# Optimization experiments

Measured on AMD Instinct MI355X. Metric: run time of the kernel, lower is better.

## Reference

```python
import jax, jax.numpy as jnp
import numpy as np

N, F, RBF, E = 50000, 128, 20, 800000
LOG2 = float(np.log(2.0))

def setup_inputs() -> dict:
    key = jax.random.key(0)
    ks = jax.random.split(key, 12)
    s = jax.random.normal(ks[0], (N, F), dtype=jnp.float32)
    v = jax.random.normal(ks[1], (N, F, 3), dtype=jnp.float32)
    edge_index = jax.random.randint(ks[2], (2, E), 0, N, dtype=jnp.int32)
    e_ij = jax.random.uniform(ks[3], (E, RBF), dtype=jnp.float32)
    r = jax.random.normal(ks[4], (E, 3), dtype=jnp.float32)
    r_hat = r / jnp.linalg.norm(r, axis=-1, keepdims=True)
    sc = 1.0 / np.sqrt(F)
    phi_W = jax.random.normal(ks[5], (F, 3 * F), dtype=jnp.float32) * sc
    phi_b = jax.random.normal(ks[6], (3 * F,), dtype=jnp.float32) * 0.01
    f1_W = jax.random.normal(ks[7], (RBF, F), dtype=jnp.float32) * (1.0 / np.sqrt(RBF))
    f1_b = jax.random.normal(ks[8], (F,), dtype=jnp.float32) * 0.01
    f2_W = jax.random.normal(ks[9], (F, 3 * F), dtype=jnp.float32) * sc
    f2_b = jax.random.normal(ks[10], (3 * F,), dtype=jnp.float32) * 0.01
    return {"s": s, "v": v, "e_ij": e_ij, "r_hat": r_hat,
            "phi_W": phi_W, "phi_b": phi_b, "f1_W": f1_W, "f1_b": f1_b,
            "f2_W": f2_W, "f2_b": f2_b, "edge_index": edge_index}

def reference(s, v, e_ij, r_hat, phi_W, phi_b, f1_W, f1_b, f2_W, f2_b, edge_index):
    src, dst = edge_index[0], edge_index[1]
    n = s.shape[0]
    # filter_net: Linear -> shifted softplus -> Linear, per edge
    h = jax.nn.softplus(e_ij @ f1_W + f1_b) - LOG2          # (E, F)
    filt = h @ f2_W + f2_b                                   # (E, 3F)
    W_s, W_v, W_r = jnp.split(filt, 3, axis=-1)              # (E, F) each
    # phi_net on gathered destination scalar features
    phi = s[dst] @ phi_W + phi_b                             # (E, 3F)
    phi_s, phi_v, phi_r = jnp.split(phi, 3, axis=-1)         # (E, F) each
    m_s = W_s * phi_s                                        # (E, F)
    m_v = W_v[..., None] * v[dst] + (W_r * phi_r)[..., None] * r_hat[:, None, :]  # (E, F, 3)
    delta_s = jax.ops.segment_sum(m_s, src, num_segments=n)  # (N, F)
    delta_v = jax.ops.segment_sum(m_v, src, num_segments=n)  # (N, F, 3)
    return delta_s, delta_v
```

## Files before the change

### kernel.cpp

```cpp
#include <hip/hip_runtime.h>
#include <math.h>

#define NN   50000
#define FF   128
#define RBFD 20
#define EE   800000
#define C3F  384
#define TE   32
#define TN   16
#define TEH  64
#define KC   16
#define HP   36

typedef __attribute__((ext_vector_type(8))) short bhalf8;
typedef __attribute__((ext_vector_type(4))) float floatx4;

__device__ __forceinline__ float softplus_m_log2(float x) {
  float t = __expf(-fabsf(x));
  return fmaxf(x, 0.0f) + __logf(1.0f + t) - 0.6931471805599453f;
}

__device__ __forceinline__ short f2bf(float x) {
  unsigned u = __float_as_uint(x);
  u += 0x7fffu + ((u >> 16) & 1u);
  return (short)(u >> 16);
}
__device__ __forceinline__ float bflo(unsigned u) { return __uint_as_float(u << 16); }
__device__ __forceinline__ float bfhi(unsigned u) { return __uint_as_float(u & 0xffff0000u); }

__device__ __forceinline__ int pkf(int f) {
  return ((f >> 5) << 5) | ((f & 15) << 1) | ((f >> 4) & 1);
}

__global__ void hist_kernel(const int* __restrict__ edge_index, int* __restrict__ cursor) {
  int e = blockIdx.x * 256 + threadIdx.x;
  if (e < EE) atomicAdd(&cursor[edge_index[e]], 1);
}

__global__ void scan_kernel(int* __restrict__ cursor, int* __restrict__ row_start) {
  __shared__ int sums[1024];
  const int tid = threadIdx.x;
  const int CH = 49;
  int base = tid * CH;
  int vals[CH];
  int local = 0;
#pragma unroll
  for (int j = 0; j < CH; ++j) {
    int i = base + j;
    int x = (i < NN) ? cursor[i] : 0;
    vals[j] = x;
    local += x;
  }
  sums[tid] = local;
  __syncthreads();
  for (int off = 1; off < 1024; off <<= 1) {
    int v2 = (tid >= off) ? sums[tid - off] : 0;
    __syncthreads();
    sums[tid] += v2;
    __syncthreads();
  }
  int excl = sums[tid] - local;
#pragma unroll
  for (int j = 0; j < CH; ++j) {
    int i = base + j;
    if (i < NN) { row_start[i] = excl; cursor[i] = excl; }
    excl += vals[j];
  }
  if (tid == 1023) row_start[NN] = excl;
}

__global__ void fill_kernel(const int* __restrict__ edge_index, int* __restrict__ cursor,
                            int* __restrict__ perm) {
  int e = blockIdx.x * 256 + threadIdx.x;
  if (e < EE) {
    int s = edge_index[e];
    int pos = atomicAdd(&cursor[s], 1);
    perm[pos] = e;
  }
}

__global__ void fill2_kernel(const int* __restrict__ edge_index, int* __restrict__ cursor,
                             int* __restrict__ perm, int* __restrict__ dst_perm) {
  int e = blockIdx.x * 256 + threadIdx.x;
  if (e < EE) {
    int s = edge_index[e];
    int d = edge_index[EE + e];
    int pos = atomicAdd(&cursor[s], 1);
    perm[pos] = e;
    dst_perm[pos] = d;
  }
}

__global__ void rperm_kernel(const float* __restrict__ r_hat, const int* __restrict__ perm,
                             float* __restrict__ rhp) {
  int i = blockIdx.x * 256 + threadIdx.x;
  if (i < EE) {
    int e = perm[i];
    rhp[(size_t)i * 3 + 0] = r_hat[(size_t)e * 3 + 0];
    rhp[(size_t)i * 3 + 1] = r_hat[(size_t)e * 3 + 1];
    rhp[(size_t)i * 3 + 2] = r_hat[(size_t)e * 3 + 2];
  }
}

__global__ void conv_kernel(const float* __restrict__ f1_W, const float* __restrict__ f2_W,
                            short* __restrict__ f1t, short* __restrict__ f2t) {
  int i = blockIdx.x * 256 + threadIdx.x;
  if (i < C3F * FF) {
    int n = i >> 7, k = i & 127;
    f2t[i] = f2bf(f2_W[(size_t)k * C3F + n]);
  }
  if (i < FF * 40) {
    int f = i / 40, k = i - f * 40;
    f1t[i] = (k < RBFD) ? f2bf(f1_W[(size_t)k * FF + f]) : (short)0;
  }
}

__global__ void vconv_kernel(const float* __restrict__ v, short* __restrict__ v_b16) {
  int i = blockIdx.x * 256 + threadIdx.x;
  if (i < NN * FF * 3) {
    int n = i / 384;
    int rem = i - n * 384;
    int f = rem / 3;
    int c = rem - f * 3;
    int g = f >> 5, l = f & 15, h = (f >> 4) & 1;
    v_b16[(size_t)n * 384 + g * 96 + l * 6 + c * 2 + h] = f2bf(v[i]);
  }
}

__global__ __launch_bounds__(256, 2)
void phi_kernel(const float* __restrict__ s, const float* __restrict__ phi_W,
                const float* __restrict__ phi_b, short* __restrict__ phi_b16) {
  __shared__ float s_t[FF * HP];
  __shared__ __align__(16) float w_ch[KC * 256];
  const int tid = threadIdx.x;
  const int r0 = blockIdx.x * TE;

  for (int i = tid; i < TE * (FF / 4); i += 256) {
    int row = i >> 5, k4 = i & 31;
    int rg = r0 + row;
    float4 sv = make_float4(0.f, 0.f, 0.f, 0.f);
    if (rg < NN) sv = *(const float4*)(s + (size_t)rg * FF + k4 * 4);
    s_t[(k4 * 4 + 0) * HP + row] = sv.x;
    s_t[(k4 * 4 + 1) * HP + row] = sv.y;
    s_t[(k4 * 4 + 2) * HP + row] = sv.z;
    s_t[(k4 * 4 + 3) * HP + row] = sv.w;
  }
  const int tc = tid & 31, tr = tid >> 5;
  float acc[2][4][4];
#pragma unroll
  for (int g = 0; g < 2; ++g)
#pragma unroll
    for (int a = 0; a < 4; ++a)
#pragma unroll
      for (int b = 0; b < 4; ++b) acc[g][a][b] = 0.f;

  for (int kc = 0; kc < FF / KC; ++kc) {
    __syncthreads();
    for (int i = tid; i < KC * 64; i += 256) {
      int k = i >> 6, j4 = i & 63;
      int j = j4 * 4;
      int col = (j < 128) ? j : (j + 128);
      *(float4*)&w_ch[k * 256 + j] =
          *(const float4*)(phi_W + (size_t)(kc * KC + k) * C3F + col);
    }
    __syncthreads();
#pragma unroll
    for (int k = 0; k < KC; ++k) {
      float4 s4 = *(const float4*)&s_t[(kc * KC + k) * HP + tr * 4];
      float sr[4] = {s4.x, s4.y, s4.z, s4.w};
#pragma unroll
      for (int g = 0; g < 2; ++g) {
        float4 w4 = *(const float4*)&w_ch[k * 256 + g * 128 + tc * 4];
        float wr[4] = {w4.x, w4.y, w4.z, w4.w};
#pragma unroll
        for (int er = 0; er < 4; ++er)
#pragma unroll
          for (int fc = 0; fc < 4; ++fc) acc[g][er][fc] += sr[er] * wr[fc];
      }
    }
  }
  const int f0 = tc * 4;
  float4 b0 = *(const float4*)(phi_b + f0);
  float4 b2 = *(const float4*)(phi_b + 256 + f0);
  float bb[2][4] = {{b0.x, b0.y, b0.z, b0.w}, {b2.x, b2.y, b2.z, b2.w}};

  __syncthreads();
  short* ob = (short*)w_ch;
#pragma unroll
  for (int er = 0; er < 4; ++er) {
    int row = tr * 4 + er;
#pragma unroll
    for (int g = 0; g < 2; ++g) {
#pragma unroll
      for (int fc = 0; fc < 4; ++fc) {
        int f = f0 + fc;
        ob[row * 256 + g * 128 + pkf(f)] = f2bf(acc[g][er][fc] + bb[g][fc]);
      }
    }
  }
  __syncthreads();
  for (int i = tid; i < 1024; i += 256) {
    int row = i >> 5;
    int rg = r0 + row;
    if (rg < NN)
      ((int4*)(phi_b16 + (size_t)rg * 256))[i & 31] = ((const int4*)ob)[i];
  }
}

__global__ __launch_bounds__(256, 6)
void h_kernel(const float* __restrict__ e_ij, const float* __restrict__ f1_b,
              const int* __restrict__ perm, const short* __restrict__ f1t_g,
              short* __restrict__ h_perm) {
  __shared__ __align__(16) short e_pad2[TEH * 40];
  __shared__ int pl[TEH];
  const int tid = threadIdx.x;
  const int wid = tid >> 6;
  const int lane = tid & 63;
  const int l = lane & 15;
  const int q = lane >> 4;
  const int e0 = blockIdx.x * TEH;

  if (tid < TEH) {
    int idx = e0 + tid;
    pl[tid] = (idx < EE) ? perm[idx] : -1;
  }
  __syncthreads();
  for (int i = tid; i < TEH * 32; i += 256) {
    int e = i >> 5, k = i & 31;
    int eid = pl[e];
    float val = (eid >= 0 && k < RBFD) ? e_ij[(size_t)eid * RBFD + k] : 0.f;
    e_pad2[e * 40 + k] = f2bf(val);
  }
  const int f0 = wid * 32 + l;
  const int f1 = f0 + 16;
  const bhalf8 b1f0 = *(const bhalf8*)(f1t_g + f0 * 40 + q * 8);
  const bhalf8 b1f1 = *(const bhalf8*)(f1t_g + f1 * 40 + q * 8);
  const float f1b0 = f1_b[f0], f1b1 = f1_b[f1];
  __syncthreads();

#pragma unroll
  for (int rt = 0; rt < 4; ++rt) {
    bhalf8 a = *(const bhalf8*)(&e_pad2[(rt * 16 + l) * 40 + q * 8]);
    floatx4 h0 = {0.f, 0.f, 0.f, 0.f}, h1 = {0.f, 0.f, 0.f, 0.f};
    h0 = __builtin_amdgcn_mfma_f32_16x16x32_bf16(a, b1f0, h0, 0, 0, 0);
    h1 = __builtin_amdgcn_mfma_f32_16x16x32_bf16(a, b1f1, h1, 0, 0, 0);
#pragma unroll
    for (int r = 0; r < 4; ++r) {
      int idx = e0 + rt * 16 + q * 4 + r;
      if (idx < EE) {
        h_perm[(size_t)idx * FF + f0] = f2bf(softplus_m_log2(h0[r] + f1b0));
        h_perm[(size_t)idx * FF + f1] = f2bf(softplus_m_log2(h1[r] + f1b1));
      }
    }
  }
}

__global__ __launch_bounds__(256, 3)
void node2_kernel(const short* __restrict__ v_b16, const float* __restrict__ rhp,
                  const float* __restrict__ f2_b,
                  const int* __restrict__ row_start, const int* __restrict__ dst_perm,
                  const short* __restrict__ phi_b16, const short* __restrict__ h_perm,
                  const short* __restrict__ f2t_g,
                  float* __restrict__ out_s, float* __restrict__ out_v) {
  const int tid = threadIdx.x;
  const int wid = tid >> 6;
  const int lane = tid & 63;
  const int l = lane & 15;
  const int q = lane >> 4;
  const int f0 = wid * 32 + l;
  const int f1 = f0 + 16;

  const float bs0 = f2_b[f0],        bs1 = f2_b[f1];
  const float bv0 = f2_b[FF + f0],   bv1 = f2_b[FF + f1];
  const float br0 = f2_b[2*FF + f0], br1 = f2_b[2*FF + f1];

  bhalf8 Bfr[6][4];
#pragma unroll
  for (int j = 0; j < 6; ++j) {
    int g = j >> 1, hh = j & 1;
    int nc = g * 128 + wid * 32 + hh * 16 + l;
#pragma unroll
    for (int ks = 0; ks < 4; ++ks)
      Bfr[j][ks] = *(const bhalf8*)(f2t_g + (size_t)nc * FF + ks * 32 + q * 8);
  }

  for (int n = blockIdx.x; n < NN; n += gridDim.x) {
    const int rs = row_start[n];
    const int deg = row_start[n + 1] - rs;

    float dsA[2] = {0.f, 0.f};
    float dvA[2][3] = {{0.f, 0.f, 0.f}, {0.f, 0.f, 0.f}};

    for (int c0 = 0; c0 < deg; c0 += TN) {
      const int cnt = min(TN, deg - c0);
      const int base = rs + c0;

      int dg[4];
#pragma unroll
      for (int r = 0; r < 4; ++r) {
        int idx = min(base + q * 4 + r, EE - 1);
        dg[r] = dst_perm[idx];
      }

      unsigned psu[4], pru[4], vu0[4], vu1[4], vu2[4];
#pragma unroll
      for (int r = 0; r < 4; ++r) {
        const short* pb = phi_b16 + (size_t)dg[r] * 256 + wid * 32 + l * 2;
        psu[r] = *(const unsigned*)pb;
        pru[r] = *(const unsigned*)(pb + 128);
        const short* vb = v_b16 + (size_t)dg[r] * 384 + wid * 96 + l * 6;
        vu0[r] = ((const unsigned*)vb)[0];
        vu1[r] = ((const unsigned*)vb)[1];
        vu2[r] = ((const unsigned*)vb)[2];
      }

      const int hrow = min(base + l, EE - 1);
      const short* hp = h_perm + (size_t)hrow * FF + q * 8;
      floatx4 acc[6];
#pragma unroll
      for (int j = 0; j < 6; ++j) acc[j] = (floatx4){0.f, 0.f, 0.f, 0.f};
#pragma unroll
      for (int ks = 0; ks < 4; ++ks) {
        bhalf8 a = *(const bhalf8*)(hp + ks * 32);
#pragma unroll
        for (int j = 0; j < 6; ++j)
          acc[j] = __builtin_amdgcn_mfma_f32_16x16x32_bf16(a, Bfr[j][ks], acc[j], 0, 0, 0);
      }

#pragma unroll
      for (int r = 0; r < 4; ++r) {
        int e = q * 4 + r;
        float valid = (e < cnt) ? 1.0f : 0.0f;
        float Ws0 = (acc[0][r] + bs0) * valid, Ws1 = (acc[1][r] + bs1) * valid;
        float Wv0 = (acc[2][r] + bv0) * valid, Wv1 = (acc[3][r] + bv1) * valid;
        float Wr0 = (acc[4][r] + br0) * valid, Wr1 = (acc[5][r] + br1) * valid;

        float ps0 = bflo(psu[r]), ps1 = bfhi(psu[r]);
        float pr0 = bflo(pru[r]), pr1 = bfhi(pru[r]);
        float v00 = bflo(vu0[r]), v10 = bfhi(vu0[r]);
        float v01 = bflo(vu1[r]), v11 = bfhi(vu1[r]);
        float v02 = bflo(vu2[r]), v12 = bfhi(vu2[r]);

        int ridx = min(base + e, EE - 1);
        const float* rp = rhp + (size_t)ridx * 3;
        float rh0 = rp[0], rh1 = rp[1], rh2 = rp[2];

        dsA[0] += Ws0 * ps0;
        dsA[1] += Ws1 * ps1;
        float w0 = Wr0 * pr0, w1 = Wr1 * pr1;
        dvA[0][0] += Wv0 * v00 + w0 * rh0;
        dvA[0][1] += Wv0 * v01 + w0 * rh1;
        dvA[0][2] += Wv0 * v02 + w0 * rh2;
        dvA[1][0] += Wv1 * v10 + w1 * rh0;
        dvA[1][1] += Wv1 * v11 + w1 * rh1;
        dvA[1][2] += Wv1 * v12 + w1 * rh2;
      }
    }

#pragma unroll
    for (int a = 0; a < 2; ++a) {
      dsA[a] += __shfl_xor(dsA[a], 16);
      dsA[a] += __shfl_xor(dsA[a], 32);
#pragma unroll
      for (int c = 0; c < 3; ++c) {
        dvA[a][c] += __shfl_xor(dvA[a][c], 16);
        dvA[a][c] += __shfl_xor(dvA[a][c], 32);
      }
    }

    if (q == 0) {
      out_s[(size_t)n * FF + f0] = dsA[0];
      out_s[(size_t)n * FF + f1] = dsA[1];
#pragma unroll
      for (int c = 0; c < 3; ++c) {
        out_v[((size_t)n * FF + f0) * 3 + c] = dvA[0][c];
        out_v[((size_t)n * FF + f1) * 3 + c] = dvA[1][c];
      }
    }
  }
}

template <bool VB16>
__global__ __launch_bounds__(256, 3)
void node_mfma_kernel(const float* __restrict__ vf32, const short* __restrict__ v_b16,
                      const float* __restrict__ e_ij, const float* __restrict__ r_hat,
                      const float* __restrict__ f1_b, const float* __restrict__ f2_b,
                      const int* __restrict__ edge_index,
                      const int* __restrict__ row_start, const int* __restrict__ perm,
                      const short* __restrict__ phi_b16,
                      const short* __restrict__ f1t_g, const short* __restrict__ f2t_g,
                      float* __restrict__ out_s, float* __restrict__ out_v) {
  __shared__ __align__(16) short f1t_l[FF * 40];
  __shared__ __align__(16) short e_pad[TN * 40];
  __shared__ __align__(16) short h_buf[TN * 136];
  __shared__ float rh_l[TN * 3];
  __shared__ int el[TN], dl[TN];

  const int tid = threadIdx.x;
  const int wid = tid >> 6;
  const int lane = tid & 63;
  const int l = lane & 15;
  const int q = lane >> 4;

  for (int i = tid; i < FF * 40 / 2; i += 256)
    ((int*)f1t_l)[i] = ((const int*)f1t_g)[i];

  const int f0 = wid * 32 + l;
  const int f1 = f0 + 16;

  const float f1b0 = f1_b[f0], f1b1 = f1_b[f1];
  const float bs0 = f2_b[f0],        bs1 = f2_b[f1];
  const float bv0 = f2_b[FF + f0],   bv1 = f2_b[FF + f1];
  const float br0 = f2_b[2*FF + f0], br1 = f2_b[2*FF + f1];

  bhalf8 Bfr[6][4];
#pragma unroll
  for (int j = 0; j < 6; ++j) {
    int g = j >> 1, hh = j & 1;
    int nc = g * 128 + wid * 32 + hh * 16 + l;
#pragma unroll
    for (int ks = 0; ks < 4; ++ks)
      Bfr[j][ks] = *(const bhalf8*)(f2t_g + (size_t)nc * FF + ks * 32 + q * 8);
  }

  __syncthreads();
  const bhalf8 b1f0 = *(const bhalf8*)(&f1t_l[f0 * 40 + q * 8]);
  const bhalf8 b1f1 = *(const bhalf8*)(&f1t_l[f1 * 40 + q * 8]);

  for (int n = blockIdx.x; n < NN; n += gridDim.x) {
    const int rs = row_start[n];
    const int deg = row_start[n + 1] - rs;

    float dsA[2] = {0.f, 0.f};
    float dvA[2][3] = {{0.f, 0.f, 0.f}, {0.f, 0.f, 0.f}};

    for (int c0 = 0; c0 < deg; c0 += TN) {
      const int cnt = min(TN, deg - c0);
      __syncthreads();

      if (tid < TN) {
        int idx = c0 + tid;
        int eid = (idx < deg) ? perm[rs + idx] : -1;
        el[tid] = eid;
        dl[tid] = (eid >= 0) ? edge_index[EE + eid] : 0;
        if (eid >= 0) {
          rh_l[tid * 3 + 0] = r_hat[(size_t)eid * 3 + 0];
          rh_l[tid * 3 + 1] = r_hat[(size_t)eid * 3 + 1];
          rh_l[tid * 3 + 2] = r_hat[(size_t)eid * 3 + 2];
        } else {
          rh_l[tid * 3 + 0] = 0.f; rh_l[tid * 3 + 1] = 0.f; rh_l[tid * 3 + 2] = 0.f;
        }
      }
      __syncthreads();
      for (int i = tid; i < TN * 32; i += 256) {
        int e = i >> 5, k = i & 31;
        int eid = el[e];
        float val = (eid >= 0 && k < RBFD) ? e_ij[(size_t)eid * RBFD + k] : 0.f;
        e_pad[e * 40 + k] = f2bf(val);
      }
      __syncthreads();

      {
        bhalf8 a = *(const bhalf8*)(&e_pad[l * 40 + q * 8]);
        floatx4 h0 = {0.f, 0.f, 0.f, 0.f}, h1 = {0.f, 0.f, 0.f, 0.f};
        h0 = __builtin_amdgcn_mfma_f32_16x16x32_bf16(a, b1f0, h0, 0, 0, 0);
        h1 = __builtin_amdgcn_mfma_f32_16x16x32_bf16(a, b1f1, h1, 0, 0, 0);
#pragma unroll
        for (int r = 0; r < 4; ++r) {
          int e = q * 4 + r;
          h_buf[e * 136 + f0] = f2bf(softplus_m_log2(h0[r] + f1b0));
          h_buf[e * 136 + f1] = f2bf(softplus_m_log2(h1[r] + f1b1));
        }
      }
      __syncthreads();

      floatx4 acc[6];
#pragma unroll
      for (int j = 0; j < 6; ++j) acc[j] = (floatx4){0.f, 0.f, 0.f, 0.f};
#pragma unroll
      for (int ks = 0; ks < 4; ++ks) {
        bhalf8 a = *(const bhalf8*)(&h_buf[l * 136 + ks * 32 + q * 8]);
#pragma unroll
        for (int j = 0; j < 6; ++j)
          acc[j] = __builtin_amdgcn_mfma_f32_16x16x32_bf16(a, Bfr[j][ks], acc[j], 0, 0, 0);
      }

#pragma unroll
      for (int r = 0; r < 4; ++r) {
        int e = q * 4 + r;
        int dg = dl[e];
        float valid = (e < cnt) ? 1.0f : 0.0f;
        float Ws0 = (acc[0][r] + bs0) * valid, Ws1 = (acc[1][r] + bs1) * valid;
        float Wv0 = (acc[2][r] + bv0) * valid, Wv1 = (acc[3][r] + bv1) * valid;
        float Wr0 = (acc[4][r] + br0) * valid, Wr1 = (acc[5][r] + br1) * valid;

        const short* pb = phi_b16 + (size_t)dg * 256 + wid * 32 + l * 2;
        unsigned psu = *(const unsigned*)pb;
        unsigned pru = *(const unsigned*)(pb + 128);
        float ps0 = bflo(psu), ps1 = bfhi(psu);
        float pr0 = bflo(pru), pr1 = bfhi(pru);

        float v00, v01, v02, v10, v11, v12;
        if constexpr (VB16) {
          const short* vb = v_b16 + (size_t)dg * 384 + wid * 96 + l * 6;
          unsigned u0 = ((const unsigned*)vb)[0];
          unsigned u1 = ((const unsigned*)vb)[1];
          unsigned u2 = ((const unsigned*)vb)[2];
          v00 = bflo(u0); v10 = bfhi(u0);
          v01 = bflo(u1); v11 = bfhi(u1);
          v02 = bflo(u2); v12 = bfhi(u2);
        } else {
          const float* vp0 = vf32 + ((size_t)dg * FF + f0) * 3;
          const float* vp1 = vf32 + ((size_t)dg * FF + f1) * 3;
          v00 = vp0[0]; v01 = vp0[1]; v02 = vp0[2];
          v10 = vp1[0]; v11 = vp1[1]; v12 = vp1[2];
        }
        float rh0 = rh_l[e * 3 + 0], rh1 = rh_l[e * 3 + 1], rh2 = rh_l[e * 3 + 2];
        dsA[0] += Ws0 * ps0;
        dsA[1] += Ws1 * ps1;
        float w0 = Wr0 * pr0, w1 = Wr1 * pr1;
        dvA[0][0] += Wv0 * v00 + w0 * rh0;
        dvA[0][1] += Wv0 * v01 + w0 * rh1;
        dvA[0][2] += Wv0 * v02 + w0 * rh2;
        dvA[1][0] += Wv1 * v10 + w1 * rh0;
        dvA[1][1] += Wv1 * v11 + w1 * rh1;
        dvA[1][2] += Wv1 * v12 + w1 * rh2;
      }
    }

#pragma unroll
    for (int a = 0; a < 2; ++a) {
      dsA[a] += __shfl_xor(dsA[a], 16);
      dsA[a] += __shfl_xor(dsA[a], 32);
#pragma unroll
      for (int c = 0; c < 3; ++c) {
        dvA[a][c] += __shfl_xor(dvA[a][c], 16);
        dvA[a][c] += __shfl_xor(dvA[a][c], 32);
      }
    }

    __syncthreads();
    float* ob = (float*)h_buf;
    if (q == 0) {
      ob[f0] = dsA[0];
      ob[f1] = dsA[1];
#pragma unroll
      for (int c = 0; c < 3; ++c) {
        ob[128 + f0 * 3 + c] = dvA[0][c];
        ob[128 + f1 * 3 + c] = dvA[1][c];
      }
    }
    __syncthreads();
    if (tid < 32)
      ((float4*)(out_s + (size_t)n * FF))[tid] = ((const float4*)ob)[tid];
    else if (tid < 128)
      ((float4*)(out_v + (size_t)n * C3F))[tid - 32] = ((const float4*)ob)[tid];
  }
}

__global__ __launch_bounds__(256, 2)
void edge_kernel(const float* __restrict__ sfeat, const float* __restrict__ v,
                 const float* __restrict__ e_ij, const float* __restrict__ r_hat,
                 const float* __restrict__ phi_W, const float* __restrict__ phi_b,
                 const float* __restrict__ f1_W, const float* __restrict__ f1_b,
                 const float* __restrict__ f2_W, const float* __restrict__ f2_b,
                 const int* __restrict__ edge_index,
                 float* __restrict__ out_s, float* __restrict__ out_v) {
  __shared__ float h_t[FF * HP];
  __shared__ float w_ch[KC * C3F];
  __shared__ float e_t[TE * RBFD];
  __shared__ float f1_lds[RBFD * FF];
  __shared__ int src_lds[TE], dst_lds[TE];
  __shared__ float rh_lds[TE * 3];
  __shared__ float s_t[FF * HP];

  const int tid = threadIdx.x;
  const int e0 = blockIdx.x * TE;

  if (tid < TE) {
    src_lds[tid] = edge_index[e0 + tid];
    dst_lds[tid] = edge_index[EE + e0 + tid];
  }
  if (tid < TE * 3) rh_lds[tid] = r_hat[(size_t)e0 * 3 + tid];
  for (int i = tid; i < TE * RBFD; i += 256) e_t[i] = e_ij[(size_t)e0 * RBFD + i];
  for (int i = tid; i < RBFD * FF; i += 256) f1_lds[i] = f1_W[i];
  __syncthreads();

  for (int i = tid; i < TE * FF; i += 256) {
    int e = i >> 7, f = i & 127;
    float x = f1_b[f];
#pragma unroll
    for (int k = 0; k < RBFD; ++k) x += e_t[e * RBFD + k] * f1_lds[k * FF + f];
    h_t[f * HP + e] = softplus_m_log2(x);
  }
  for (int i = tid; i < TE * (FF / 4); i += 256) {
    int e = i >> 5, k4 = i & 31;
    int d = dst_lds[e];
    float4 sv = *(const float4*)(sfeat + (size_t)d * FF + k4 * 4);
    s_t[(k4 * 4 + 0) * HP + e] = sv.x;
    s_t[(k4 * 4 + 1) * HP + e] = sv.y;
    s_t[(k4 * 4 + 2) * HP + e] = sv.z;
    s_t[(k4 * 4 + 3) * HP + e] = sv.w;
  }

  const int tc = tid & 31, tr = tid >> 5;
  float facc[3][4][4];
  float pacc[2][4][4];
#pragma unroll
  for (int g = 0; g < 3; ++g)
#pragma unroll
    for (int a = 0; a < 4; ++a)
#pragma unroll
      for (int b = 0; b < 4; ++b) facc[g][a][b] = 0.f;
#pragma unroll
  for (int g = 0; g < 2; ++g)
#pragma unroll
    for (int a = 0; a < 4; ++a)
#pragma unroll
      for (int b = 0; b < 4; ++b) pacc[g][a][b] = 0.f;

  for (int kc = 0; kc < FF / KC; ++kc) {
    __syncthreads();
    for (int i = tid; i < KC * C3F / 4; i += 256)
      *(float4*)&w_ch[i * 4] =
          *(const float4*)(f2_W + (size_t)kc * KC * C3F + i * 4);
    __syncthreads();
#pragma unroll
    for (int k = 0; k < KC; ++k) {
      float4 h4 = *(const float4*)&h_t[(kc * KC + k) * HP + tr * 4];
      float hr[4] = {h4.x, h4.y, h4.z, h4.w};
#pragma unroll
      for (int g = 0; g < 3; ++g) {
        float4 w4 = *(const float4*)&w_ch[k * C3F + g * 128 + tc * 4];
        float wr[4] = {w4.x, w4.y, w4.z, w4.w};
#pragma unroll
        for (int er = 0; er < 4; ++er)
#pragma unroll
          for (int fc = 0; fc < 4; ++fc) facc[g][er][fc] += hr[er] * wr[fc];
      }
    }
  }

  for (int kc = 0; kc < FF / KC; ++kc) {
    __syncthreads();
    for (int i = tid; i < KC * 64; i += 256) {
      int k = i >> 6, j4 = i & 63;
      int j = j4 * 4;
      int col = (j < 128) ? j : (j + 128);
      *(float4*)&w_ch[k * C3F + j] =
          *(const float4*)(phi_W + (size_t)(kc * KC + k) * C3F + col);
    }
    __syncthreads();
#pragma unroll
    for (int k = 0; k < KC; ++k) {
      float4 s4 = *(const float4*)&s_t[(kc * KC + k) * HP + tr * 4];
      float sr[4] = {s4.x, s4.y, s4.z, s4.w};
#pragma unroll
      for (int g = 0; g < 2; ++g) {
        float4 w4 = *(const float4*)&w_ch[k * C3F + g * 128 + tc * 4];
        float wr[4] = {w4.x, w4.y, w4.z, w4.w};
#pragma unroll
        for (int er = 0; er < 4; ++er)
#pragma unroll
          for (int fc = 0; fc < 4; ++fc) pacc[g][er][fc] += sr[er] * wr[fc];
      }
    }
  }

  const int f0 = tc * 4;
  float4 bs4 = *(const float4*)(f2_b + f0);
  float4 bv4 = *(const float4*)(f2_b + FF + f0);
  float4 br4 = *(const float4*)(f2_b + 2 * FF + f0);
  float bs[4] = {bs4.x, bs4.y, bs4.z, bs4.w};
  float bv[4] = {bv4.x, bv4.y, bv4.z, bv4.w};
  float br[4] = {br4.x, br4.y, br4.z, br4.w};
  float4 p0b = *(const float4*)(phi_b + f0);
  float4 p2b = *(const float4*)(phi_b + 256 + f0);
  float pb0[4] = {p0b.x, p0b.y, p0b.z, p0b.w};
  float pb2[4] = {p2b.x, p2b.y, p2b.z, p2b.w};

#pragma unroll
  for (int er = 0; er < 4; ++er) {
    const int e = tr * 4 + er;
    const int sg = src_lds[e];
    const int dg = dst_lds[e];
    const float r0c = rh_lds[e * 3 + 0];
    const float r1c = rh_lds[e * 3 + 1];
    const float r2c = rh_lds[e * 3 + 2];

    float ps[4], pr[4];
#pragma unroll
    for (int fc = 0; fc < 4; ++fc) {
      ps[fc] = pacc[0][er][fc] + pb0[fc];
      pr[fc] = pacc[1][er][fc] + pb2[fc];
    }

    float pv[12];
    const float* vp = v + ((size_t)dg * FF + f0) * 3;
    float4 v0 = *(const float4*)(vp);
    float4 v1 = *(const float4*)(vp + 4);
    float4 v2 = *(const float4*)(vp + 8);
    pv[0] = v0.x; pv[1] = v0.y; pv[2] = v0.z; pv[3] = v0.w;
    pv[4] = v1.x; pv[5] = v1.y; pv[6] = v1.z; pv[7] = v1.w;
    pv[8] = v2.x; pv[9] = v2.y; pv[10] = v2.z; pv[11] = v2.w;

    float* os = out_s + (size_t)sg * FF + f0;
    float* ov = out_v + ((size_t)sg * FF + f0) * 3;
#pragma unroll
    for (int fc = 0; fc < 4; ++fc) {
      float Ws = facc[0][er][fc] + bs[fc];
      float Wv = facc[1][er][fc] + bv[fc];
      float Wr = facc[2][er][fc] + br[fc];
      atomicAdd(os + fc, Ws * ps[fc]);
      float wrp = Wr * pr[fc];
      atomicAdd(ov + fc * 3 + 0, Wv * pv[fc * 3 + 0] + wrp * r0c);
      atomicAdd(ov + fc * 3 + 1, Wv * pv[fc * 3 + 1] + wrp * r1c);
      atomicAdd(ov + fc * 3 + 2, Wv * pv[fc * 3 + 2] + wrp * r2c);
    }
  }
}

extern "C" void kernel_launch(void* const* d_in, const int* in_sizes, int n_in,
                              void* d_out, int out_size, void* d_ws, size_t ws_size,
                              hipStream_t stream) {
  const float* s      = (const float*)d_in[0];
  const float* v      = (const float*)d_in[1];
  const float* e_ij   = (const float*)d_in[2];
  const float* r_hat  = (const float*)d_in[3];
  const float* phi_W  = (const float*)d_in[4];
  const float* phi_b  = (const float*)d_in[5];
  const float* f1_W   = (const float*)d_in[6];
  const float* f1_b   = (const float*)d_in[7];
  const float* f2_W   = (const float*)d_in[8];
  const float* f2_b   = (const float*)d_in[9];
  const int* edge_index = (const int*)d_in[10];

  float* out = (float*)d_out;
  float* out_s = out;
  float* out_v = out + (size_t)NN * FF;

  {
    int*   row_start = (int*)d_ws;
    int*   cursor    = row_start + 50008;
    int*   perm      = cursor + NN;
    int*   dst_perm  = perm + EE;
    float* rhp       = (float*)(dst_perm + EE);
    short* phi_b16   = (short*)(rhp + (size_t)EE * 3);
    short* f2t       = phi_b16 + (size_t)NN * 256;
    short* f1t       = f2t + C3F * FF;
    short* v_b16     = f1t + FF * 40;
    short* h_perm    = v_b16 + (size_t)NN * 384;
    const size_t huge_bytes =
        (size_t)(50008 + NN + EE + EE) * 4 + (size_t)EE * 3 * 4 +
        ((size_t)NN * 256 + (size_t)C3F * FF + (size_t)FF * 40 +
         (size_t)NN * 384 + (size_t)EE * FF) * 2;

    if (ws_size >= huge_bytes) {
      hipMemsetAsync(cursor, 0, (size_t)NN * sizeof(int), stream);
      hist_kernel<<<(EE + 255) / 256, 256, 0, stream>>>(edge_index, cursor);
      scan_kernel<<<1, 1024, 0, stream>>>(cursor, row_start);
      fill2_kernel<<<(EE + 255) / 256, 256, 0, stream>>>(edge_index, cursor, perm, dst_perm);
      conv_kernel<<<(C3F * FF + 255) / 256, 256, 0, stream>>>(f1_W, f2_W, f1t, f2t);
      phi_kernel<<<(NN + TE - 1) / TE, 256, 0, stream>>>(s, phi_W, phi_b, phi_b16);
      rperm_kernel<<<(EE + 255) / 256, 256, 0, stream>>>(r_hat, perm, rhp);
      vconv_kernel<<<(NN * 384 + 255) / 256, 256, 0, stream>>>(v, v_b16);
      h_kernel<<<(EE + TEH - 1) / TEH, 256, 0, stream>>>(e_ij, f1_b, perm, f1t, h_perm);
      node2_kernel<<<768, 256, 0, stream>>>(v_b16, rhp, f2_b, row_start, dst_perm,
                                            phi_b16, h_perm, f2t, out_s, out_v);
      return;
    }
  }

  int* row_start = (int*)d_ws;
  int* cursor    = row_start + 50008;
  int* perm      = cursor + NN;
  short* phi_b16 = (short*)(perm + EE);
  short* f2t     = phi_b16 + (size_t)NN * 256;
  short* f1t     = f2t + C3F * FF;
  short* v_b16   = f1t + FF * 40;
  const size_t mid_bytes  = (size_t)(50008 + NN + EE) * 4 +
                            ((size_t)NN * 256 + C3F * FF + FF * 40) * 2;
  const size_t full_bytes = mid_bytes + (size_t)NN * 384 * 2;

  if (ws_size >= mid_bytes) {
    hipMemsetAsync(cursor, 0, (size_t)NN * sizeof(int), stream);
    hist_kernel<<<(EE + 255) / 256, 256, 0, stream>>>(edge_index, cursor);
    scan_kernel<<<1, 1024, 0, stream>>>(cursor, row_start);
    fill_kernel<<<(EE + 255) / 256, 256, 0, stream>>>(edge_index, cursor, perm);
    conv_kernel<<<(C3F * FF + 255) / 256, 256, 0, stream>>>(f1_W, f2_W, f1t, f2t);
    phi_kernel<<<(NN + TE - 1) / TE, 256, 0, stream>>>(s, phi_W, phi_b, phi_b16);
    if (ws_size >= full_bytes) {
      vconv_kernel<<<(NN * 384 + 255) / 256, 256, 0, stream>>>(v, v_b16);
      node_mfma_kernel<true><<<768, 256, 0, stream>>>(
          v, v_b16, e_ij, r_hat, f1_b, f2_b, edge_index, row_start, perm,
          phi_b16, f1t, f2t, out_s, out_v);
    } else {
      node_mfma_kernel<false><<<768, 256, 0, stream>>>(
          v, nullptr, e_ij, r_hat, f1_b, f2_b, edge_index, row_start, perm,
          phi_b16, f1t, f2t, out_s, out_v);
    }
  } else {
    hipMemsetAsync(d_out, 0, (size_t)out_size * sizeof(float), stream);
    edge_kernel<<<EE / TE, 256, 0, stream>>>(
        s, v, e_ij, r_hat, phi_W, phi_b, f1_W, f1_b, f2_W, f2_b, edge_index,
        out_s, out_v);
  }
}
```

Before: 1.215 ms.

## Fuse r_hat permutation into h_kernel, pack vconv writes, one block per node

```diff
diff --git a/kernel.cpp b/kernel.cpp
--- a/kernel.cpp
+++ b/kernel.cpp
@@ -91,17 +91,6 @@
   }
 }
 
-__global__ void rperm_kernel(const float* __restrict__ r_hat, const int* __restrict__ perm,
-                             float* __restrict__ rhp) {
-  int i = blockIdx.x * 256 + threadIdx.x;
-  if (i < EE) {
-    int e = perm[i];
-    rhp[(size_t)i * 3 + 0] = r_hat[(size_t)e * 3 + 0];
-    rhp[(size_t)i * 3 + 1] = r_hat[(size_t)e * 3 + 1];
-    rhp[(size_t)i * 3 + 2] = r_hat[(size_t)e * 3 + 2];
-  }
-}
-
 __global__ void conv_kernel(const float* __restrict__ f1_W, const float* __restrict__ f2_W,
                             short* __restrict__ f1t, short* __restrict__ f2t) {
   int i = blockIdx.x * 256 + threadIdx.x;
@@ -117,17 +106,22 @@
 
 __global__ void vconv_kernel(const float* __restrict__ v, short* __restrict__ v_b16) {
   int i = blockIdx.x * 256 + threadIdx.x;
-  if (i < NN * FF * 3) {
-    int n = i / 384;
-    int rem = i - n * 384;
-    int f = rem / 3;
-    int c = rem - f * 3;
-    int g = f >> 5, l = f & 15, h = (f >> 4) & 1;
-    v_b16[(size_t)n * 384 + g * 96 + l * 6 + c * 2 + h] = f2bf(v[i]);
-  }
-}
-
-__global__ __launch_bounds__(256, 2)
+  if (i < NN * 192) {
+    int n = i / 192;
+    int rem = i - n * 192;
+    int g = rem / 48;
+    int w = rem - g * 48;
+    int l = w / 3;
+    int c = w - l * 3;
+    float v0 = v[((size_t)n * FF + g * 32 + l) * 3 + c];
+    float v1 = v[((size_t)n * FF + g * 32 + 16 + l) * 3 + c];
+    unsigned word = (unsigned)(unsigned short)f2bf(v0) |
+                    ((unsigned)(unsigned short)f2bf(v1) << 16);
+    ((unsigned*)v_b16)[(size_t)n * 192 + rem] = word;
+  }
+}
+
+__global__ __launch_bounds__(256, 3)
 void phi_kernel(const float* __restrict__ s, const float* __restrict__ phi_W,
                 const float* __restrict__ phi_b, short* __restrict__ phi_b16) {
   __shared__ float s_t[FF * HP];
@@ -209,8 +203,9 @@
 
 __global__ __launch_bounds__(256, 6)
 void h_kernel(const float* __restrict__ e_ij, const float* __restrict__ f1_b,
+              const float* __restrict__ r_hat,
               const int* __restrict__ perm, const short* __restrict__ f1t_g,
-              short* __restrict__ h_perm) {
+              short* __restrict__ h_perm, float* __restrict__ rhp) {
   __shared__ __align__(16) short e_pad2[TEH * 40];
   __shared__ int pl[TEH];
   const int tid = threadIdx.x;
@@ -225,6 +220,14 @@
     pl[tid] = (idx < EE) ? perm[idx] : -1;
   }
   __syncthreads();
+  if (tid < TEH * 3) {
+    int le = tid / 3, c = tid - le * 3;
+    int idx = e0 + le;
+    if (idx < EE) {
+      int eid = pl[le];
+      rhp[(size_t)idx * 3 + c] = (eid >= 0) ? r_hat[(size_t)eid * 3 + c] : 0.f;
+    }
+  }
   for (int i = tid; i < TEH * 32; i += 256) {
     int e = i >> 5, k = i & 31;
     int eid = pl[e];
@@ -284,98 +287,97 @@
       Bfr[j][ks] = *(const bhalf8*)(f2t_g + (size_t)nc * FF + ks * 32 + q * 8);
   }
 
-  for (int n = blockIdx.x; n < NN; n += gridDim.x) {
-    const int rs = row_start[n];
-    const int deg = row_start[n + 1] - rs;
-
-    float dsA[2] = {0.f, 0.f};
-    float dvA[2][3] = {{0.f, 0.f, 0.f}, {0.f, 0.f, 0.f}};
-
-    for (int c0 = 0; c0 < deg; c0 += TN) {
-      const int cnt = min(TN, deg - c0);
-      const int base = rs + c0;
-
-      int dg[4];
-#pragma unroll
-      for (int r = 0; r < 4; ++r) {
-        int idx = min(base + q * 4 + r, EE - 1);
-        dg[r] = dst_perm[idx];
-      }
-
-      unsigned psu[4], pru[4], vu0[4], vu1[4], vu2[4];
-#pragma unroll
-      for (int r = 0; r < 4; ++r) {
-        const short* pb = phi_b16 + (size_t)dg[r] * 256 + wid * 32 + l * 2;
-        psu[r] = *(const unsigned*)pb;
-        pru[r] = *(const unsigned*)(pb + 128);
-        const short* vb = v_b16 + (size_t)dg[r] * 384 + wid * 96 + l * 6;
-        vu0[r] = ((const unsigned*)vb)[0];
-        vu1[r] = ((const unsigned*)vb)[1];
-        vu2[r] = ((const unsigned*)vb)[2];
-      }
-
-      const int hrow = min(base + l, EE - 1);
-      const short* hp = h_perm + (size_t)hrow * FF + q * 8;
-      floatx4 acc[6];
-#pragma unroll
-      for (int j = 0; j < 6; ++j) acc[j] = (floatx4){0.f, 0.f, 0.f, 0.f};
-#pragma unroll
-      for (int ks = 0; ks < 4; ++ks) {
-        bhalf8 a = *(const bhalf8*)(hp + ks * 32);
-#pragma unroll
-        for (int j = 0; j < 6; ++j)
-          acc[j] = __builtin_amdgcn_mfma_f32_16x16x32_bf16(a, Bfr[j][ks], acc[j], 0, 0, 0);
-      }
-
-#pragma unroll
-      for (int r = 0; r < 4; ++r) {
-        int e = q * 4 + r;
-        float valid = (e < cnt) ? 1.0f : 0.0f;
-        float Ws0 = (acc[0][r] + bs0) * valid, Ws1 = (acc[1][r] + bs1) * valid;
-        float Wv0 = (acc[2][r] + bv0) * valid, Wv1 = (acc[3][r] + bv1) * valid;
-        float Wr0 = (acc[4][r] + br0) * valid, Wr1 = (acc[5][r] + br1) * valid;
-
-        float ps0 = bflo(psu[r]), ps1 = bfhi(psu[r]);
-        float pr0 = bflo(pru[r]), pr1 = bfhi(pru[r]);
-        float v00 = bflo(vu0[r]), v10 = bfhi(vu0[r]);
-        float v01 = bflo(vu1[r]), v11 = bfhi(vu1[r]);
-        float v02 = bflo(vu2[r]), v12 = bfhi(vu2[r]);
-
-        int ridx = min(base + e, EE - 1);
-        const float* rp = rhp + (size_t)ridx * 3;
-        float rh0 = rp[0], rh1 = rp[1], rh2 = rp[2];
-
-        dsA[0] += Ws0 * ps0;
-        dsA[1] += Ws1 * ps1;
-        float w0 = Wr0 * pr0, w1 = Wr1 * pr1;
-        dvA[0][0] += Wv0 * v00 + w0 * rh0;
-        dvA[0][1] += Wv0 * v01 + w0 * rh1;
-        dvA[0][2] += Wv0 * v02 + w0 * rh2;
-        dvA[1][0] += Wv1 * v10 + w1 * rh0;
-        dvA[1][1] += Wv1 * v11 + w1 * rh1;
-        dvA[1][2] += Wv1 * v12 + w1 * rh2;
-      }
-    }
-
-#pragma unroll
-    for (int a = 0; a < 2; ++a) {
-      dsA[a] += __shfl_xor(dsA[a], 16);
-      dsA[a] += __shfl_xor(dsA[a], 32);
-#pragma unroll
-      for (int c = 0; c < 3; ++c) {
-        dvA[a][c] += __shfl_xor(dvA[a][c], 16);
-        dvA[a][c] += __shfl_xor(dvA[a][c], 32);
-      }
-    }
-
-    if (q == 0) {
-      out_s[(size_t)n * FF + f0] = dsA[0];
-      out_s[(size_t)n * FF + f1] = dsA[1];
-#pragma unroll
-      for (int c = 0; c < 3; ++c) {
-        out_v[((size_t)n * FF + f0) * 3 + c] = dvA[0][c];
-        out_v[((size_t)n * FF + f1) * 3 + c] = dvA[1][c];
-      }
+  const int n = blockIdx.x;
+  const int rs = row_start[n];
+  const int deg = row_start[n + 1] - rs;
+
+  float dsA[2] = {0.f, 0.f};
+  float dvA[2][3] = {{0.f, 0.f, 0.f}, {0.f, 0.f, 0.f}};
+
+  for (int c0 = 0; c0 < deg; c0 += TN) {
+    const int cnt = min(TN, deg - c0);
+    const int base = rs + c0;
+
+    int dg[4];
+#pragma unroll
+    for (int r = 0; r < 4; ++r) {
+      int idx = min(base + q * 4 + r, EE - 1);
+      dg[r] = dst_perm[idx];
+    }
+
+    unsigned psu[4], pru[4], vu0[4], vu1[4], vu2[4];
+#pragma unroll
+    for (int r = 0; r < 4; ++r) {
+      const short* pb = phi_b16 + (size_t)dg[r] * 256 + wid * 32 + l * 2;
+      psu[r] = *(const unsigned*)pb;
+      pru[r] = *(const unsigned*)(pb + 128);
+      const short* vb = v_b16 + (size_t)dg[r] * 384 + wid * 96 + l * 6;
+      vu0[r] = ((const unsigned*)vb)[0];
+      vu1[r] = ((const unsigned*)vb)[1];
+      vu2[r] = ((const unsigned*)vb)[2];
+    }
+
+    const int hrow = min(base + l, EE - 1);
+    const short* hp = h_perm + (size_t)hrow * FF + q * 8;
+    floatx4 acc[6];
+#pragma unroll
+    for (int j = 0; j < 6; ++j) acc[j] = (floatx4){0.f, 0.f, 0.f, 0.f};
+#pragma unroll
+    for (int ks = 0; ks < 4; ++ks) {
+      bhalf8 a = *(const bhalf8*)(hp + ks * 32);
+#pragma unroll
+      for (int j = 0; j < 6; ++j)
+        acc[j] = __builtin_amdgcn_mfma_f32_16x16x32_bf16(a, Bfr[j][ks], acc[j], 0, 0, 0);
+    }
+
+#pragma unroll
+    for (int r = 0; r < 4; ++r) {
+      int e = q * 4 + r;
+      float valid = (e < cnt) ? 1.0f : 0.0f;
+      float Ws0 = (acc[0][r] + bs0) * valid, Ws1 = (acc[1][r] + bs1) * valid;
+      float Wv0 = (acc[2][r] + bv0) * valid, Wv1 = (acc[3][r] + bv1) * valid;
+      float Wr0 = (acc[4][r] + br0) * valid, Wr1 = (acc[5][r] + br1) * valid;
+
+      float ps0 = bflo(psu[r]), ps1 = bfhi(psu[r]);
+      float pr0 = bflo(pru[r]), pr1 = bfhi(pru[r]);
+      float v00 = bflo(vu0[r]), v10 = bfhi(vu0[r]);
+      float v01 = bflo(vu1[r]), v11 = bfhi(vu1[r]);
+      float v02 = bflo(vu2[r]), v12 = bfhi(vu2[r]);
+
+      int ridx = min(base + e, EE - 1);
+      const float* rp = rhp + (size_t)ridx * 3;
+      float rh0 = rp[0], rh1 = rp[1], rh2 = rp[2];
+
+      dsA[0] += Ws0 * ps0;
+      dsA[1] += Ws1 * ps1;
+      float w0 = Wr0 * pr0, w1 = Wr1 * pr1;
+      dvA[0][0] += Wv0 * v00 + w0 * rh0;
+      dvA[0][1] += Wv0 * v01 + w0 * rh1;
+      dvA[0][2] += Wv0 * v02 + w0 * rh2;
+      dvA[1][0] += Wv1 * v10 + w1 * rh0;
+      dvA[1][1] += Wv1 * v11 + w1 * rh1;
+      dvA[1][2] += Wv1 * v12 + w1 * rh2;
+    }
+  }
+
+#pragma unroll
+  for (int a = 0; a < 2; ++a) {
+    dsA[a] += __shfl_xor(dsA[a], 16);
+    dsA[a] += __shfl_xor(dsA[a], 32);
+#pragma unroll
+    for (int c = 0; c < 3; ++c) {
+      dvA[a][c] += __shfl_xor(dvA[a][c], 16);
+      dvA[a][c] += __shfl_xor(dvA[a][c], 32);
+    }
+  }
+
+  if (q == 0) {
+    out_s[(size_t)n * FF + f0] = dsA[0];
+    out_s[(size_t)n * FF + f1] = dsA[1];
+#pragma unroll
+    for (int c = 0; c < 3; ++c) {
+      out_v[((size_t)n * FF + f0) * 3 + c] = dvA[0][c];
+      out_v[((size_t)n * FF + f1) * 3 + c] = dvA[1][c];
     }
   }
 }
@@ -762,11 +764,11 @@
       fill2_kernel<<<(EE + 255) / 256, 256, 0, stream>>>(edge_index, cursor, perm, dst_perm);
       conv_kernel<<<(C3F * FF + 255) / 256, 256, 0, stream>>>(f1_W, f2_W, f1t, f2t);
       phi_kernel<<<(NN + TE - 1) / TE, 256, 0, stream>>>(s, phi_W, phi_b, phi_b16);
-      rperm_kernel<<<(EE + 255) / 256, 256, 0, stream>>>(r_hat, perm, rhp);
-      vconv_kernel<<<(NN * 384 + 255) / 256, 256, 0, stream>>>(v, v_b16);
-      h_kernel<<<(EE + TEH - 1) / TEH, 256, 0, stream>>>(e_ij, f1_b, perm, f1t, h_perm);
-      node2_kernel<<<768, 256, 0, stream>>>(v_b16, rhp, f2_b, row_start, dst_perm,
-                                            phi_b16, h_perm, f2t, out_s, out_v);
+      vconv_kernel<<<(NN * 192 + 255) / 256, 256, 0, stream>>>(v, v_b16);
+      h_kernel<<<(EE + TEH - 1) / TEH, 256, 0, stream>>>(e_ij, f1_b, r_hat, perm, f1t,
+                                                         h_perm, rhp);
+      node2_kernel<<<NN, 256, 0, stream>>>(v_b16, rhp, f2_b, row_start, dst_perm,
+                                           phi_b16, h_perm, f2t, out_s, out_v);
       return;
     }
   }
@@ -790,7 +792,7 @@
     conv_kernel<<<(C3F * FF + 255) / 256, 256, 0, stream>>>(f1_W, f2_W, f1t, f2t);
     phi_kernel<<<(NN + TE - 1) / TE, 256, 0, stream>>>(s, phi_W, phi_b, phi_b16);
     if (ws_size >= full_bytes) {
-      vconv_kernel<<<(NN * 384 + 255) / 256, 256, 0, stream>>>(v, v_b16);
+      vconv_kernel<<<(NN * 192 + 255) / 256, 256, 0, stream>>>(v, v_b16);
       node_mfma_kernel<true><<<768, 256, 0, stream>>>(
           v, v_b16, e_ij, r_hat, f1_b, f2_b, edge_index, row_start, perm,
           phi_b16, f1t, f2t, out_s, out_v);
```

Measured after the change: 1.606 ms. +32.2%, slower.
